# Optimization experiments

Measured on AMD Instinct MI355X. Metric: run time of the kernel, lower is better.

## Reference

```python
import jax, jax.numpy as jnp
import numpy as np

D = 512
H = 512


def setup_inputs() -> dict:
    key = jax.random.key(0)
    k1, k2, k3, k4 = jax.random.split(key, 4)
    N, T = 64, 1024
    x = jax.random.normal(k1, (N, T, D), dtype=jnp.float32)
    h0 = jax.random.normal(k2, (N, H), dtype=jnp.float32)
    Wx = jax.random.normal(k3, (D, 4 * H), dtype=jnp.float32) / jnp.sqrt(jnp.float32(D))
    Wh = jax.random.normal(k4, (H, 4 * H), dtype=jnp.float32) / jnp.sqrt(jnp.float32(H))
    b = jnp.zeros((4 * H,), dtype=jnp.float32)
    return {"x": x, "h0": h0, "Wx": Wx, "Wh": Wh, "b": b}


def reference(x, h0, Wx, Wh, b):
    # x: (N, T, D), h0: (N, H). Returns hn: (N, T, H).
    N, T, _ = x.shape
    Hdim = h0.shape[1]
    # Input projection is independent of the recurrence: hoist out of the scan.
    xW = jnp.einsum('ntd,df->ntf', x, Wx) + b  # (N, T, 4H)
    xW_t = jnp.swapaxes(xW, 0, 1)  # (T, N, 4H)

    def step(carry, xw_t):
        h, c = carry
        a = xw_t + h @ Wh  # (N, 4H)
        i, f, o, g = jnp.split(a, 4, axis=1)
        i = jax.nn.sigmoid(i)
        f = jax.nn.sigmoid(f)
        o = jax.nn.sigmoid(o)
        g = jnp.tanh(g)
        c_next = f * c + i * g
        h_next = o * jnp.tanh(c_next)
        return (h_next, c_next), h_next

    c0 = jnp.zeros_like(h0)
    _, hs = jax.lax.scan(step, (h0, c0), xW_t)  # hs: (T, N, H)
    return jnp.swapaxes(hs, 0, 1)  # (N, T, H)
```

## Files before the change

### kernel.cpp

```cpp
#include <hip/hip_runtime.h>


#define TT 1024
#define NB 64
#define DD 512
#define HH 512
#define XROW 520
#define NBHH (NB * HH)
#define TTDD (TT * DD)

typedef _Float16 half8 __attribute__((ext_vector_type(8)));
typedef _Float16 half4 __attribute__((ext_vector_type(4)));
typedef float floatx4 __attribute__((ext_vector_type(4)));
typedef unsigned long long u64;
typedef unsigned int u32;
typedef unsigned short u16;

#define AQ __ATOMIC_RELAXED
#define SC __HIP_MEMORY_SCOPE_AGENT

__global__ void init_ws_kernel(u64* hq) {
    hq[blockIdx.x * 256 + threadIdx.x] = 0x0000FFFF0000FFFFULL;
}

__device__ __forceinline__ void barrier_lgkm() {
    asm volatile("s_waitcnt lgkmcnt(0)" ::: "memory");
    __builtin_amdgcn_s_barrier();
    asm volatile("" ::: "memory");
}

#define MFMA16(A, B, C) __builtin_amdgcn_mfma_f32_16x16x32_f16((A), (B), (C), 0, 0, 0)

__global__ __launch_bounds__(256, 1) void lstm_persist(
    const float* __restrict__ x, const float* __restrict__ h0,
    const float* __restrict__ Wx, const float* __restrict__ Wh,
    const float* __restrict__ b, float* __restrict__ out,
    u64* __restrict__ hq)
{
    const int tid  = threadIdx.x;
    const int lane = tid & 63;
    const int wave = tid >> 6;
    const int cg   = blockIdx.x & 31;
    const int rg   = blockIdx.x >> 5;
    const int row0 = rg << 4;

    __shared__ __align__(16) _Float16 xbuf[2][16 * XROW];
    __shared__ __align__(16) _Float16 hlds[16 * XROW];
    __shared__ float gatebuf[4 * 272];
    __shared__ float houts[2][128];

    const int bcol = (wave << 9) + (cg << 4) + (lane & 15);
    const int kq   = (lane >> 4) << 3;
    half8 bfrag[32];
#pragma unroll
    for (int kt = 0; kt < 16; ++kt)
#pragma unroll
        for (int j = 0; j < 8; ++j)
            bfrag[kt][j] = (_Float16)Wx[(size_t)((kt << 5) + kq + j) * 2048 + bcol];
#pragma unroll
    for (int kt = 16; kt < 32; ++kt)
#pragma unroll
        for (int j = 0; j < 8; ++j)
            bfrag[kt][j] = (_Float16)Wh[(size_t)((kt << 5) + kq + j - 512) * 2048 + bcol];

    const int tr = tid >> 4;
    const int tc = tid & 15;
    const int gn = row0 + tr;
    const int gh = (cg << 4) + tc;
    const float bi = b[0 * 512 + gh];
    const float bf = b[1 * 512 + gh];
    const float bo = b[2 * 512 + gh];
    const float bg = b[3 * 512 + gh];
    float c_state = 0.f;

    const int r2 = tid >> 7;
    const int d4 = tid & 127;
    const int arow = (lane & 15) * XROW + kq;

    const int lt  = tid & 127;
    const int xr  = lt >> 3;
    const int xc8 = lt & 7;

#pragma unroll
    for (int i = 0; i < 8; ++i) {
        int r = (i << 1) + r2;
        float4 xv = ((const float4*)(x + (size_t)(row0 + r) * TTDD))[d4];
        half4 hc;
        hc.x = (_Float16)xv.x; hc.y = (_Float16)xv.y;
        hc.z = (_Float16)xv.z; hc.w = (_Float16)xv.w;
        *(half4*)&xbuf[0][r * XROW + (d4 << 2)] = hc;
    }
    {
        float hv0 = h0[(size_t)gn * HH + gh];
        float pn  = __shfl_down(hv0, 1);
        if ((tc & 1) == 0) {
            _Float16 f0 = (_Float16)hv0, f1 = (_Float16)pn;
            u16 b0, b1;
            __builtin_memcpy(&b0, &f0, 2); __builtin_memcpy(&b1, &f1, 2);
            const u32 wtag = 0xB000u;
            u32 lo = ((u32)b0 << 16) | wtag;
            u32 hi = ((u32)b1 << 16) | wtag;
            u64 v = (u64)lo | ((u64)hi << 32);
            __hip_atomic_store(hq + (size_t)gn * 256 + (gh >> 1), v, AQ, SC);
        }
    }
    barrier_lgkm();

    for (int t = 0; t < TT; ++t) {
        const bool havex = (t + 1 < TT);

        float4 xvv[16];
        if (wave >= 2 && havex) {
            const float4* xsrc = (const float4*)(x + (size_t)(row0 + xr) * TTDD
                                                 + (size_t)(t + 1) * DD);
#pragma unroll
            for (int j = 0; j < 16; ++j)
                xvv[j] = xsrc[xc8 + (j << 3)];
        }

        floatx4 acc0 = {0.f, 0.f, 0.f, 0.f};
        floatx4 acc1 = {0.f, 0.f, 0.f, 0.f};
        const _Float16* xa = xbuf[t & 1];
#pragma unroll
        for (int kt = 0; kt < 16; kt += 2) {
            half8 a0 = *(const half8*)&xa[arow + (kt << 5)];
            half8 a1 = *(const half8*)&xa[arow + ((kt + 1) << 5)];
            acc0 = MFMA16(a0, bfrag[kt],     acc0);
            acc1 = MFMA16(a1, bfrag[kt + 1], acc1);
        }

        if (wave < 2) {
            const int pr = tid >> 3;
            const int pc = tid & 7;
            const u64 wantp = ((u64)(0xB000u | ((u32)(t >> 1) & 1u)))
                              * 0x0000000100000001ULL;
            const u64* src = hq + (size_t)(t & 1) * (NBHH / 2)
                           + (size_t)(row0 + pr) * 256 + pc;
            u64 w[32];
            bool ok;
            do {
#pragma unroll
                for (int j = 0; j < 32; ++j)
                    w[j] = __hip_atomic_load(src + (j << 3), AQ, SC);
                u64 chk = 0;
#pragma unroll
                for (int j = 0; j < 32; ++j)
                    chk |= (w[j] ^ wantp) & 0x0000FFFF0000FFFFULL;
                ok = (chk == 0);
            } while (!ok);
            u32* dst = (u32*)hlds + pr * 260 + pc;
#pragma unroll
            for (int j = 0; j < 32; ++j) {
                u32 lo = (u32)w[j] >> 16;
                u32 hi = (u32)(w[j] >> 32) & 0xFFFF0000u;
                dst[j << 3] = lo | hi;
            }
        }
        barrier_lgkm();

#pragma unroll
        for (int kt = 0; kt < 16; kt += 2) {
            half8 a0 = *(const half8*)&hlds[arow + (kt << 5)];
            half8 a1 = *(const half8*)&hlds[arow + ((kt + 1) << 5)];
            acc0 = MFMA16(a0, bfrag[16 + kt],     acc0);
            acc1 = MFMA16(a1, bfrag[16 + kt + 1], acc1);
        }
        floatx4 acc = acc0 + acc1;

        {
            const int ccol = lane & 15;
            const int crow = (lane >> 4) << 2;
#pragma unroll
            for (int v = 0; v < 4; ++v)
                gatebuf[wave * 272 + (crow + v) * 17 + ccol] = acc[v];
        }

        if (wave >= 2) {
            if (t > 0) {
                float hvp = houts[(t - 1) & 1][lt];
                out[(size_t)(row0 + (lt >> 4)) * (TT * HH) + (size_t)(t - 1) * HH
                    + (cg << 4) + (lt & 15)] = hvp;
            }
            if (havex) {
                _Float16* xd = xbuf[(t + 1) & 1] + xr * XROW;
                half4 hc;
#pragma unroll
                for (int j = 0; j < 16; ++j) {
                    float4 v = xvv[j];
                    hc.x = (_Float16)v.x; hc.y = (_Float16)v.y;
                    hc.z = (_Float16)v.z; hc.w = (_Float16)v.w;
                    *(half4*)&xd[(xc8 + (j << 3)) << 2] = hc;
                }
            }
        }
        barrier_lgkm();

        {
            const int gidx = tr * 17 + tc;
            float ai = gatebuf[0 * 272 + gidx] + bi;
            float af = gatebuf[1 * 272 + gidx] + bf;
            float ao = gatebuf[2 * 272 + gidx] + bo;
            float ag = gatebuf[3 * 272 + gidx] + bg;
            float ig = 1.f / (1.f + __expf(-ai));
            float fg = 1.f / (1.f + __expf(-af));
            float og = 1.f / (1.f + __expf(-ao));
            float gg = 2.f / (1.f + __expf(-2.f * ag)) - 1.f;
            c_state = fg * c_state + ig * gg;
            float hv = og * (2.f / (1.f + __expf(-2.f * c_state)) - 1.f);

            float pn = __shfl_down(hv, 1);
            if ((tc & 1) == 0) {
                _Float16 f0 = (_Float16)hv, f1 = (_Float16)pn;
                u16 b0, b1;
                __builtin_memcpy(&b0, &f0, 2); __builtin_memcpy(&b1, &f1, 2);
                const u32 wtag = 0xB000u | ((u32)((t + 1) >> 1) & 1u);
                u32 lo = ((u32)b0 << 16) | wtag;
                u32 hi = ((u32)b1 << 16) | wtag;
                u64 v = (u64)lo | ((u64)hi << 32);
                __hip_atomic_store(hq + (size_t)((t + 1) & 1) * (NBHH / 2)
                                   + (size_t)gn * 256 + (gh >> 1), v, AQ, SC);
            }
            if (wave < 2) houts[t & 1][tid] = hv;
            else out[(size_t)gn * (TT * HH) + (size_t)t * HH + gh] = hv;
        }
    }

    barrier_lgkm();
    if (wave >= 2) {
        float hvp = houts[(TT - 1) & 1][lt];
        out[(size_t)(row0 + (lt >> 4)) * (TT * HH) + (size_t)(TT - 1) * HH
            + (cg << 4) + (lt & 15)] = hvp;
    }
}

extern "C" void kernel_launch(void* const* d_in, const int* in_sizes, int n_in,
                              void* d_out, int out_size, void* d_ws, size_t ws_size,
                              hipStream_t stream) {
    const float* x  = (const float*)d_in[0];
    const float* h0 = (const float*)d_in[1];
    const float* Wx = (const float*)d_in[2];
    const float* Wh = (const float*)d_in[3];
    const float* b  = (const float*)d_in[4];
    float* out = (float*)d_out;

    u64* hq = (u64*)d_ws;

    init_ws_kernel<<<128, 256, 0, stream>>>(hq);
    lstm_persist<<<dim3(128), dim3(256), 0, stream>>>(x, h0, Wx, Wh, b, out, hq);
}
```

Before: 3.091 ms.

## Use 64 blocks of 512 threads with 32 hidden columns per block

```diff
diff --git a/kernel.cpp b/kernel.cpp
--- a/kernel.cpp
+++ b/kernel.cpp
@@ -31,7 +31,7 @@
 
 #define MFMA16(A, B, C) __builtin_amdgcn_mfma_f32_16x16x32_f16((A), (B), (C), 0, 0, 0)
 
-__global__ __launch_bounds__(256, 1) void lstm_persist(
+__global__ __launch_bounds__(512, 1) void lstm_persist(
     const float* __restrict__ x, const float* __restrict__ h0,
     const float* __restrict__ Wx, const float* __restrict__ Wh,
     const float* __restrict__ b, float* __restrict__ out,
@@ -40,16 +40,18 @@
     const int tid  = threadIdx.x;
     const int lane = tid & 63;
     const int wave = tid >> 6;
-    const int cg   = blockIdx.x & 31;
-    const int rg   = blockIdx.x >> 5;
+    const int gate = wave & 3;
+    const int ch   = wave >> 2;
+    const int cg   = blockIdx.x & 15;
+    const int rg   = blockIdx.x >> 4;
     const int row0 = rg << 4;
 
     __shared__ __align__(16) _Float16 xbuf[2][16 * XROW];
     __shared__ __align__(16) _Float16 hlds[16 * XROW];
-    __shared__ float gatebuf[4 * 272];
-    __shared__ float houts[2][128];
-
-    const int bcol = (wave << 9) + (cg << 4) + (lane & 15);
+    __shared__ float gatebuf[4 * 16 * 33];
+    __shared__ float houts[2][256];
+
+    const int bcol = (gate << 9) + (cg << 5) + (ch << 4) + (lane & 15);
     const int kq   = (lane >> 4) << 3;
     half8 bfrag[32];
 #pragma unroll
@@ -63,37 +65,41 @@
         for (int j = 0; j < 8; ++j)
             bfrag[kt][j] = (_Float16)Wh[(size_t)((kt << 5) + kq + j - 512) * 2048 + bcol];
 
-    const int tr = tid >> 4;
-    const int tc = tid & 15;
-    const int gn = row0 + tr;
-    const int gh = (cg << 4) + tc;
+    const int er = tid >> 5;
+    const int ec = tid & 31;
+    const int gn = row0 + er;
+    const int gh = (cg << 5) + ec;
     const float bi = b[0 * 512 + gh];
     const float bf = b[1 * 512 + gh];
     const float bo = b[2 * 512 + gh];
     const float bg = b[3 * 512 + gh];
     float c_state = 0.f;
 
-    const int r2 = tid >> 7;
-    const int d4 = tid & 127;
+    const bool isx = tid >= 256;
+    const int pr = (tid >> 4) & 15;
+    const int pc = tid & 15;
+    const int xtid = tid & 255;
+    const int xr = xtid >> 4;
+    const int xc = xtid & 15;
+
     const int arow = (lane & 15) * XROW + kq;
 
-    const int lt  = tid & 127;
-    const int xr  = lt >> 3;
-    const int xc8 = lt & 7;
-
-#pragma unroll
-    for (int i = 0; i < 8; ++i) {
-        int r = (i << 1) + r2;
-        float4 xv = ((const float4*)(x + (size_t)(row0 + r) * TTDD))[d4];
-        half4 hc;
-        hc.x = (_Float16)xv.x; hc.y = (_Float16)xv.y;
-        hc.z = (_Float16)xv.z; hc.w = (_Float16)xv.w;
-        *(half4*)&xbuf[0][r * XROW + (d4 << 2)] = hc;
+    if (isx) {
+        const float4* xs = (const float4*)(x + (size_t)(row0 + xr) * TTDD);
+        _Float16* xd = xbuf[0] + xr * XROW;
+#pragma unroll
+        for (int j = 0; j < 8; ++j) {
+            float4 v = xs[xc + (j << 4)];
+            half4 hc;
+            hc.x = (_Float16)v.x; hc.y = (_Float16)v.y;
+            hc.z = (_Float16)v.z; hc.w = (_Float16)v.w;
+            *(half4*)&xd[(xc + (j << 4)) << 2] = hc;
+        }
     }
     {
         float hv0 = h0[(size_t)gn * HH + gh];
         float pn  = __shfl_down(hv0, 1);
-        if ((tc & 1) == 0) {
+        if ((ec & 1) == 0) {
             _Float16 f0 = (_Float16)hv0, f1 = (_Float16)pn;
             u16 b0, b1;
             __builtin_memcpy(&b0, &f0, 2); __builtin_memcpy(&b1, &f1, 2);
@@ -109,13 +115,13 @@
     for (int t = 0; t < TT; ++t) {
         const bool havex = (t + 1 < TT);
 
-        float4 xvv[16];
-        if (wave >= 2 && havex) {
+        float4 xvv[8];
+        if (isx && havex) {
             const float4* xsrc = (const float4*)(x + (size_t)(row0 + xr) * TTDD
                                                  + (size_t)(t + 1) * DD);
 #pragma unroll
-            for (int j = 0; j < 16; ++j)
-                xvv[j] = xsrc[xc8 + (j << 3)];
+            for (int j = 0; j < 8; ++j)
+                xvv[j] = xsrc[xc + (j << 4)];
         }
 
         floatx4 acc0 = {0.f, 0.f, 0.f, 0.f};
@@ -129,34 +135,36 @@
             acc1 = MFMA16(a1, bfrag[kt + 1], acc1);
         }
 
-        if (wave < 2) {
-            const int pr = tid >> 3;
-            const int pc = tid & 7;
+        if (!isx) {
             const u64 wantp = ((u64)(0xB000u | ((u32)(t >> 1) & 1u)))
                               * 0x0000000100000001ULL;
             const u64* src = hq + (size_t)(t & 1) * (NBHH / 2)
                            + (size_t)(row0 + pr) * 256 + pc;
-            u64 w[32];
-            bool ok;
+            u64 w[16];
+            unsigned rdy = 0;
             do {
 #pragma unroll
-                for (int j = 0; j < 32; ++j)
-                    w[j] = __hip_atomic_load(src + (j << 3), AQ, SC);
-                u64 chk = 0;
-#pragma unroll
-                for (int j = 0; j < 32; ++j)
-                    chk |= (w[j] ^ wantp) & 0x0000FFFF0000FFFFULL;
-                ok = (chk == 0);
-            } while (!ok);
+                for (int j = 0; j < 16; ++j)
+                    if (!((rdy >> j) & 1u))
+                        w[j] = __hip_atomic_load(src + (j << 4), AQ, SC);
+#pragma unroll
+                for (int j = 0; j < 16; ++j)
+                    if (!((rdy >> j) & 1u)
+                        && ((w[j] ^ wantp) & 0x0000FFFF0000FFFFULL) == 0)
+                        rdy |= 1u << j;
+            } while (rdy != 0xFFFFu);
             u32* dst = (u32*)hlds + pr * 260 + pc;
 #pragma unroll
-            for (int j = 0; j < 32; ++j) {
+            for (int j = 0; j < 16; ++j) {
                 u32 lo = (u32)w[j] >> 16;
                 u32 hi = (u32)(w[j] >> 32) & 0xFFFF0000u;
-                dst[j << 3] = lo | hi;
+                dst[j << 4] = lo | hi;
             }
         }
         barrier_lgkm();
+
+        float hprev = 0.f;
+        if (isx && t > 0) hprev = houts[(t - 1) & 1][xtid];
 
 #pragma unroll
         for (int kt = 0; kt < 16; kt += 2) {
@@ -168,39 +176,38 @@
         floatx4 acc = acc0 + acc1;
 
         {
-            const int ccol = lane & 15;
+            const int ccol = (ch << 4) + (lane & 15);
             const int crow = (lane >> 4) << 2;
 #pragma unroll
             for (int v = 0; v < 4; ++v)
-                gatebuf[wave * 272 + (crow + v) * 17 + ccol] = acc[v];
-        }
-
-        if (wave >= 2) {
-            if (t > 0) {
-                float hvp = houts[(t - 1) & 1][lt];
-                out[(size_t)(row0 + (lt >> 4)) * (TT * HH) + (size_t)(t - 1) * HH
-                    + (cg << 4) + (lt & 15)] = hvp;
-            }
+                gatebuf[gate * 528 + (crow + v) * 33 + ccol] = acc[v];
+        }
+
+        if (isx) {
             if (havex) {
+                asm volatile("s_waitcnt vmcnt(0)" ::: "memory");
                 _Float16* xd = xbuf[(t + 1) & 1] + xr * XROW;
                 half4 hc;
 #pragma unroll
-                for (int j = 0; j < 16; ++j) {
+                for (int j = 0; j < 8; ++j) {
                     float4 v = xvv[j];
                     hc.x = (_Float16)v.x; hc.y = (_Float16)v.y;
                     hc.z = (_Float16)v.z; hc.w = (_Float16)v.w;
-                    *(half4*)&xd[(xc8 + (j << 3)) << 2] = hc;
+                    *(half4*)&xd[(xc + (j << 4)) << 2] = hc;
                 }
             }
+            if (t > 0) {
+                out[(size_t)(row0 + (xtid >> 5)) * (TT * HH)
+                    + (size_t)(t - 1) * HH + (cg << 5) + (xtid & 31)] = hprev;
+            }
         }
         barrier_lgkm();
 
         {
-            const int gidx = tr * 17 + tc;
-            float ai = gatebuf[0 * 272 + gidx] + bi;
-            float af = gatebuf[1 * 272 + gidx] + bf;
-            float ao = gatebuf[2 * 272 + gidx] + bo;
-            float ag = gatebuf[3 * 272 + gidx] + bg;
+            float ai = gatebuf[0 * 528 + er * 33 + ec] + bi;
+            float af = gatebuf[1 * 528 + er * 33 + ec] + bf;
+            float ao = gatebuf[2 * 528 + er * 33 + ec] + bo;
+            float ag = gatebuf[3 * 528 + er * 33 + ec] + bg;
             float ig = 1.f / (1.f + __expf(-ai));
             float fg = 1.f / (1.f + __expf(-af));
             float og = 1.f / (1.f + __expf(-ao));
@@ -209,7 +216,7 @@
             float hv = og * (2.f / (1.f + __expf(-2.f * c_state)) - 1.f);
 
             float pn = __shfl_down(hv, 1);
-            if ((tc & 1) == 0) {
+            if ((ec & 1) == 0) {
                 _Float16 f0 = (_Float16)hv, f1 = (_Float16)pn;
                 u16 b0, b1;
                 __builtin_memcpy(&b0, &f0, 2); __builtin_memcpy(&b1, &f1, 2);
@@ -220,16 +227,16 @@
                 __hip_atomic_store(hq + (size_t)((t + 1) & 1) * (NBHH / 2)
                                    + (size_t)gn * 256 + (gh >> 1), v, AQ, SC);
             }
-            if (wave < 2) houts[t & 1][tid] = hv;
+            if (!isx) houts[t & 1][tid] = hv;
             else out[(size_t)gn * (TT * HH) + (size_t)t * HH + gh] = hv;
         }
     }
 
     barrier_lgkm();
-    if (wave >= 2) {
-        float hvp = houts[(TT - 1) & 1][lt];
-        out[(size_t)(row0 + (lt >> 4)) * (TT * HH) + (size_t)(TT - 1) * HH
-            + (cg << 4) + (lt & 15)] = hvp;
+    if (isx) {
+        float hvp = houts[(TT - 1) & 1][xtid];
+        out[(size_t)(row0 + (xtid >> 5)) * (TT * HH)
+            + (size_t)(TT - 1) * HH + (cg << 5) + (xtid & 31)] = hvp;
     }
 }
 
@@ -246,5 +253,5 @@
     u64* hq = (u64*)d_ws;
 
     init_ws_kernel<<<128, 256, 0, stream>>>(hq);
-    lstm_persist<<<dim3(128), dim3(256), 0, stream>>>(x, h0, Wx, Wh, b, out, hq);
-}
+    lstm_persist<<<dim3(64), dim3(512), 0, stream>>>(x, h0, Wx, Wh, b, out, hq);
+}
```

Result: slower. 3.786 ms (+22.5%).
